# Optimization experiments

Measured on AMD Instinct MI355X. Metric: run time of the kernel, lower is better.

The kernel has to match this reference:

```python
import jax, jax.numpy as jnp
import numpy as np

B, C, H, W = 8, 512, 64, 64
C8 = C // 8

def setup_inputs() -> dict:
    key = jax.random.key(0)
    ks = jax.random.split(key, 10)
    rn = lambda k, shape: jax.random.normal(k, shape, jnp.float32)
    return {
        "q": rn(ks[0], (B, C, H, W)),
        "k": rn(ks[1], (B, C, H, W)),
        "v": rn(ks[2], (B, C, H, W)),
        "Wq": rn(ks[3], (C8, C)) * 0.05,
        "bq": rn(ks[4], (C8,)) * 0.05,
        "Wk": rn(ks[5], (C8, C)) * 0.05,
        "bk": rn(ks[6], (C8,)) * 0.05,
        "Wv": rn(ks[7], (C, C)) * 0.05,
        "bv": rn(ks[8], (C,)) * 0.05,
        "gamma": rn(ks[9], ()) * 0.05,
    }

def reference(q, k, v, Wq, bq, Wk, bk, Wv, bv, gamma):
    _, _, Hh, Ww = q.shape
    # 1x1 convs == per-pixel channel matmuls
    pq = jnp.einsum('oc,bchw->bohw', Wq, q) + bq[None, :, None, None]
    pk = jnp.einsum('oc,bchw->bohw', Wk, k) + bk[None, :, None, None]
    pv = jnp.einsum('oc,bchw->bohw', Wv, v) + bv[None, :, None, None]
    # column (height-axis) attention energies, diagonal masked to -inf
    eH = jnp.einsum('bchw,bckw->bhwk', pq, pk)  # [B,H,W,H]
    diag_mask = jnp.where(jnp.eye(Hh, dtype=bool), -jnp.inf, 0.0)  # [H,H]
    eH = eH + diag_mask[None, :, None, :]
    # row (width-axis) attention energies
    eW = jnp.einsum('bchw,bchk->bhwk', pq, pk)  # [B,H,W,W]
    # joint softmax over concatenated H+W candidates
    att = jax.nn.softmax(jnp.concatenate([eH, eW], axis=3), axis=3)
    aH, aW = att[..., :Hh], att[..., Hh:]
    outH = jnp.einsum('bckw,bhwk->bchw', pv, aH)
    outW = jnp.einsum('bchk,bhwk->bchw', pv, aW)
    return gamma * (outH + outW) + v
```

## Files before the change

### kernel.cpp

```cpp
#include <hip/hip_runtime.h>
#include <math.h>

#define Bz 8
#define Cc 512
#define Hh 64
#define Ww 64
#define HW 4096
#define BK 64
#define AS (BK + 4)
#define TS 68

typedef __attribute__((ext_vector_type(8))) short short8;
typedef __attribute__((ext_vector_type(4))) short short4v;
typedef __attribute__((ext_vector_type(4))) float floatx4;

__device__ inline unsigned short f2bf(float x) {
    unsigned u = __float_as_uint(x);
    return (unsigned short)((u + 0x7FFFu + ((u >> 16) & 1u)) >> 16);
}
__device__ inline float b2f(unsigned short h) {
    return __uint_as_float(((unsigned)h) << 16);
}
__device__ inline short8 ld8(const unsigned short* p) {
    short4v a = *(const short4v*)p;
    short4v b = *(const short4v*)(p + 4);
    short8 r;
    r[0]=a[0]; r[1]=a[1]; r[2]=a[2]; r[3]=a[3];
    r[4]=b[0]; r[5]=b[1]; r[6]=b[2]; r[7]=b[3];
    return r;
}
__device__ inline short8 ld8s(const unsigned short* base, int row, int koct) {
    return ld8(base + row * TS + (((koct ^ (row & 7))) << 3));
}

__global__ __launch_bounds__(256) void wconv_kernel(
    const float* __restrict__ Wq, const float* __restrict__ Wk,
    const float* __restrict__ Wv, unsigned short* __restrict__ wsc)
{
    const int i = blockIdx.x * 256 + threadIdx.x;
    if (i < 32768) {
        float x = Wq[i];
        unsigned short h = f2bf(x);
        wsc[i] = h;
        wsc[32768 + i] = f2bf(x - b2f(h));
    } else if (i < 65536) {
        int j = i - 32768;
        float x = Wk[j];
        unsigned short h = f2bf(x);
        wsc[65536 + j] = h;
        wsc[98304 + j] = f2bf(x - b2f(h));
    } else {
        int j = i - 65536;
        wsc[131072 + j] = f2bf(Wv[j]);
    }
}

__global__ __launch_bounds__(256, 4) void qkproj_kernel(
    const float* __restrict__ in0, const float* __restrict__ in1,
    const unsigned short* __restrict__ Wh0, const unsigned short* __restrict__ Wh1,
    const unsigned short* __restrict__ Wl0, const unsigned short* __restrict__ Wl1,
    const float* __restrict__ bias0, const float* __restrict__ bias1,
    float* __restrict__ out0, float* __restrict__ out1)
{
    __shared__ unsigned short Ah[2][64][AS];
    __shared__ unsigned short Bh[2][64][AS];
    const int sel = blockIdx.z >> 3;
    const int b   = blockIdx.z & 7;
    const float* __restrict__ in = sel ? in1 : in0;
    const unsigned short* __restrict__ Wh = sel ? Wh1 : Wh0;
    const unsigned short* __restrict__ Wl = sel ? Wl1 : Wl0;
    const float* __restrict__ bias = sel ? bias1 : bias0;
    float* __restrict__ outT = sel ? out1 : out0;

    const int t = threadIdx.x, lane = t & 63, wv = t >> 6;
    const int p0 = blockIdx.x * 64;
    const float* __restrict__ inb = in + (size_t)b * Cc * HW + p0;

    const int wm = (wv & 1) * 32;
    const int wn = (wv >> 1) * 32;

    floatx4 acc[2][2];
#pragma unroll
    for (int i = 0; i < 2; ++i)
#pragma unroll
        for (int j = 0; j < 2; ++j) acc[i][j] = (floatx4)0.f;

    const int pq4 = t & 15;
    const int cst = (t >> 4) * 4;

    for (int kt = 0; kt < Cc / BK; ++kt) {
        const int c0 = kt * BK;
        __syncthreads();
        float4 xq[4];
#pragma unroll
        for (int j = 0; j < 4; ++j)
            xq[j] = *(const float4*)(inb + (size_t)(c0 + cst + j) * HW + (pq4 << 2));
#pragma unroll
        for (int jj = 0; jj < 4; ++jj) {
            unsigned short h[4], l[4];
#pragma unroll
            for (int j = 0; j < 4; ++j) {
                float xx = ((const float*)&xq[j])[jj];
                h[j] = f2bf(xx);
                l[j] = f2bf(xx - b2f(h[j]));
            }
            *(ushort4*)&Ah[0][(pq4 << 2) + jj][cst] = make_ushort4(h[0], h[1], h[2], h[3]);
            *(ushort4*)&Ah[1][(pq4 << 2) + jj][cst] = make_ushort4(l[0], l[1], l[2], l[3]);
        }
#pragma unroll
        for (int r = 0; r < 2; ++r) {
            const int task = t + 256 * r;
            const int o = task >> 3, oct = task & 7;
            const unsigned short* srch = Wh + (size_t)o * Cc + c0 + oct * 8;
            const unsigned short* srcl = Wl + (size_t)o * Cc + c0 + oct * 8;
            *(ushort4*)&Bh[0][o][oct * 8]     = *(const ushort4*)srch;
            *(ushort4*)&Bh[0][o][oct * 8 + 4] = *(const ushort4*)(srch + 4);
            *(ushort4*)&Bh[1][o][oct * 8]     = *(const ushort4*)srcl;
            *(ushort4*)&Bh[1][o][oct * 8 + 4] = *(const ushort4*)(srcl + 4);
        }
        __syncthreads();
#pragma unroll
        for (int ks = 0; ks < 2; ++ks) {
            const int col = ks * 32 + (lane >> 4) * 8;
            short8 af[2], al[2], bfr[2], blr[2];
#pragma unroll
            for (int mt = 0; mt < 2; ++mt) {
                const int row = wm + mt * 16 + (lane & 15);
                af[mt] = ld8(&Ah[0][row][col]);
                al[mt] = ld8(&Ah[1][row][col]);
            }
#pragma unroll
            for (int nt = 0; nt < 2; ++nt) {
                const int row = wn + nt * 16 + (lane & 15);
                bfr[nt] = ld8(&Bh[0][row][col]);
                blr[nt] = ld8(&Bh[1][row][col]);
            }
#pragma unroll
            for (int mt = 0; mt < 2; ++mt)
#pragma unroll
                for (int nt = 0; nt < 2; ++nt) {
                    acc[mt][nt] = __builtin_amdgcn_mfma_f32_16x16x32_bf16(
                        af[mt], bfr[nt], acc[mt][nt], 0, 0, 0);
                    acc[mt][nt] = __builtin_amdgcn_mfma_f32_16x16x32_bf16(
                        al[mt], bfr[nt], acc[mt][nt], 0, 0, 0);
                    acc[mt][nt] = __builtin_amdgcn_mfma_f32_16x16x32_bf16(
                        af[mt], blr[nt], acc[mt][nt], 0, 0, 0);
                }
        }
    }
    const int oc = lane & 15, qd = lane >> 4;
#pragma unroll
    for (int nt = 0; nt < 2; ++nt) {
        const int o = wn + nt * 16 + oc;
        const float bs = bias[o];
#pragma unroll
        for (int mt = 0; mt < 2; ++mt)
#pragma unroll
            for (int r = 0; r < 4; ++r) {
                const int p = p0 + wm + mt * 16 + qd * 4 + r;
                outT[((size_t)b * HW + p) * 64 + o] = acc[mt][nt][r] + bs;
            }
    }
}

__global__ __launch_bounds__(256, 4) void vproj_kernel(
    const float* __restrict__ in, const unsigned short* __restrict__ Wh,
    const float* __restrict__ bias, unsigned short* __restrict__ out16)
{
    __shared__ unsigned short Ah[128][AS];
    __shared__ unsigned short Bh[128][AS];
    const int b = blockIdx.z;
    const int t = threadIdx.x, lane = t & 63, wv = t >> 6;
    const int p0 = blockIdx.x * 128, o0 = blockIdx.y * 128;
    const float* __restrict__ inb = in + (size_t)b * Cc * HW + p0;
    const int wm = (wv & 1) * 64, wn = (wv >> 1) * 64;

    floatx4 acc[4][4];
#pragma unroll
    for (int i = 0; i < 4; ++i)
#pragma unroll
        for (int j = 0; j < 4; ++j) acc[i][j] = (floatx4)0.f;

    const int pq4 = t & 31;
    const int oct = t >> 5;

    for (int kt = 0; kt < Cc / BK; ++kt) {
        const int c0 = kt * BK;
        __syncthreads();
#pragma unroll
        for (int half = 0; half < 2; ++half) {
            float4 xq[4];
#pragma unroll
            for (int j = 0; j < 4; ++j)
                xq[j] = *(const float4*)(inb + (size_t)(c0 + oct * 8 + half * 4 + j) * HW + (pq4 << 2));
#pragma unroll
            for (int jj = 0; jj < 4; ++jj) {
                unsigned short h[4];
#pragma unroll
                for (int j = 0; j < 4; ++j) h[j] = f2bf(((const float*)&xq[j])[jj]);
                *(ushort4*)&Ah[(pq4 << 2) + jj][oct * 8 + half * 4] =
                    make_ushort4(h[0], h[1], h[2], h[3]);
            }
        }
#pragma unroll
        for (int r = 0; r < 4; ++r) {
            const int task = t + 256 * r;
            const int o = task >> 3, oc8 = task & 7;
            const unsigned short* src = Wh + (size_t)(o0 + o) * Cc + c0 + oc8 * 8;
            *(ushort4*)&Bh[o][oc8 * 8]     = *(const ushort4*)src;
            *(ushort4*)&Bh[o][oc8 * 8 + 4] = *(const ushort4*)(src + 4);
        }
        __syncthreads();
#pragma unroll
        for (int ks = 0; ks < 2; ++ks) {
            const int col = ks * 32 + (lane >> 4) * 8;
            short8 af[4], bfr[4];
#pragma unroll
            for (int mt = 0; mt < 4; ++mt)
                af[mt] = ld8(&Ah[wm + mt * 16 + (lane & 15)][col]);
#pragma unroll
            for (int nt = 0; nt < 4; ++nt)
                bfr[nt] = ld8(&Bh[wn + nt * 16 + (lane & 15)][col]);
#pragma unroll
            for (int mt = 0; mt < 4; ++mt)
#pragma unroll
                for (int nt = 0; nt < 4; ++nt)
                    acc[mt][nt] = __builtin_amdgcn_mfma_f32_16x16x32_bf16(
                        af[mt], bfr[nt], acc[mt][nt], 0, 0, 0);
        }
    }
    const int oc = lane & 15, qd = lane >> 4;
#pragma unroll
    for (int nt = 0; nt < 4; ++nt) {
        const int o = o0 + wn + nt * 16 + oc;
        const float bs = bias[o];
#pragma unroll
        for (int mt = 0; mt < 4; ++mt)
#pragma unroll
            for (int r = 0; r < 4; ++r) {
                const int p = p0 + wm + mt * 16 + qd * 4 + r;
                out16[((size_t)b * HW + p) * 512 + o] = f2bf(acc[mt][nt][r] + bs);
            }
    }
}

__global__ __launch_bounds__(256) void scores_kernel(
    const float* __restrict__ pqT, const float* __restrict__ pkT,
    float* __restrict__ S)
{
    const int x    = blockIdx.x;
    const int b    = blockIdx.y;
    const int mode = blockIdx.z;
    __shared__ float Q[64][65];
    __shared__ float Kt[64][68];
    for (int idx = threadIdx.x; idx < 4096; idx += 256) {
        int r = idx >> 6, c = idx & 63;
        int p = mode ? (x * Ww + r) : (r * Ww + x);
        size_t g = ((size_t)b * HW + p) * 64 + c;
        Q[r][c] = pqT[g];
        Kt[c][r] = pkT[g];
    }
    __syncthreads();
    const int qr = threadIdx.x >> 2;
    const int k0 = (threadIdx.x & 3) * 16;
    float acc[16];
#pragma unroll
    for (int j = 0; j < 16; ++j) acc[j] = 0.f;
#pragma unroll 2
    for (int c = 0; c < 64; ++c) {
        const float qv = Q[qr][c];
        const float4 kv0 = *(const float4*)&Kt[c][k0];
        const float4 kv1 = *(const float4*)&Kt[c][k0 + 4];
        const float4 kv2 = *(const float4*)&Kt[c][k0 + 8];
        const float4 kv3 = *(const float4*)&Kt[c][k0 + 12];
        acc[0]  = fmaf(qv, kv0.x, acc[0]);
        acc[1]  = fmaf(qv, kv0.y, acc[1]);
        acc[2]  = fmaf(qv, kv0.z, acc[2]);
        acc[3]  = fmaf(qv, kv0.w, acc[3]);
        acc[4]  = fmaf(qv, kv1.x, acc[4]);
        acc[5]  = fmaf(qv, kv1.y, acc[5]);
        acc[6]  = fmaf(qv, kv1.z, acc[6]);
        acc[7]  = fmaf(qv, kv1.w, acc[7]);
        acc[8]  = fmaf(qv, kv2.x, acc[8]);
        acc[9]  = fmaf(qv, kv2.y, acc[9]);
        acc[10] = fmaf(qv, kv2.z, acc[10]);
        acc[11] = fmaf(qv, kv2.w, acc[11]);
        acc[12] = fmaf(qv, kv3.x, acc[12]);
        acc[13] = fmaf(qv, kv3.y, acc[13]);
        acc[14] = fmaf(qv, kv3.z, acc[14]);
        acc[15] = fmaf(qv, kv3.w, acc[15]);
    }
    size_t o = mode ? (((size_t)(b * Hh + x) * Ww + qr) * 128 + 64 + k0)
                    : (((size_t)(b * Hh + qr) * Ww + x) * 128 + k0);
#pragma unroll
    for (int j = 0; j < 16; ++j) S[o + j] = acc[j];
}

__global__ __launch_bounds__(256) void softmax_kernel(
    const float* __restrict__ S, unsigned short* __restrict__ Abf)
{
    const int wave = threadIdx.x >> 6;
    const int lane = threadIdx.x & 63;
    const size_t row = (size_t)blockIdx.x * 4 + wave;
    const int h = (int)((row / Ww) % Hh);
    const float* p = S + row * 128;
    float s0 = p[lane], s1 = p[lane + 64];
    if (lane == h) s0 = -INFINITY;
    float m = fmaxf(s0, s1);
#pragma unroll
    for (int off = 32; off > 0; off >>= 1) m = fmaxf(m, __shfl_xor(m, off));
    float e0 = __expf(s0 - m), e1 = __expf(s1 - m);
    float s = e0 + e1;
#pragma unroll
    for (int off = 32; off > 0; off >>= 1) s += __shfl_xor(s, off);
    float inv = 1.0f / s;
    Abf[row * 128 + lane]      = f2bf(e0 * inv);
    Abf[row * 128 + 64 + lane] = f2bf(e1 * inv);
}

__global__ __launch_bounds__(256) void outH_mfma_kernel(
    const unsigned short* __restrict__ Abf, const unsigned short* __restrict__ pvT16,
    unsigned short* __restrict__ TH16)
{
    const int w = blockIdx.x;
    const int ctg = blockIdx.y;
    const int b = blockIdx.z;
    const int t = threadIdx.x, lane = t & 63, wv = t >> 6;
    const int l15 = lane & 15, h4 = lane >> 4;
    __shared__ unsigned short A[64 * TS];
    __shared__ unsigned short Pt[64 * TS];

    {
        const int rr = t >> 2, kq = t & 3;
        const unsigned short* src = Abf + ((((size_t)b * Hh + rr) * Ww + w) << 7) + kq * 16;
        ushort4 a0 = *(const ushort4*)(src);
        ushort4 a1 = *(const ushort4*)(src + 4);
        ushort4 a2 = *(const ushort4*)(src + 8);
        ushort4 a3 = *(const ushort4*)(src + 12);
        const int sw = (rr & 7) << 3;
        const int q0 = rr * TS + (((kq * 2) << 3) ^ sw);
        const int q1 = rr * TS + (((kq * 2 + 1) << 3) ^ sw);
        *(ushort4*)&A[q0] = a0; *(ushort4*)&A[q0 + 4] = a1;
        *(ushort4*)&A[q1] = a2; *(ushort4*)&A[q1 + 4] = a3;
    }
    __syncthreads();
    const int hm = (wv & 1) * 32, cn = (wv >> 1) * 32;
    short8 ah[2][2];
#pragma unroll
    for (int mt = 0; mt < 2; ++mt)
#pragma unroll
        for (int ks = 0; ks < 2; ++ks)
            ah[mt][ks] = ld8s(A, hm + mt * 16 + l15, ks * 4 + h4);

    for (int cc = 0; cc < 2; ++cc) {
        const int cbase = (ctg * 2 + cc) * 64;
        __syncthreads();
        {
            const int kp = t >> 3, co = t & 7, k0 = kp * 2;
            const unsigned short* s0 = pvT16 + (((size_t)b * HW + (size_t)k0 * Ww + w) << 9) + cbase + co * 8;
            const unsigned short* s1 = s0 + ((size_t)Ww << 9);
            short8 r0 = *(const short8*)s0;
            short8 r1 = *(const short8*)s1;
            const int oct = k0 >> 3, klo = k0 & 7;
#pragma unroll
            for (int j = 0; j < 8; ++j) {
                const int c = co * 8 + j;
                unsigned vv = (unsigned)(unsigned short)r0[j] | ((unsigned)(unsigned short)r1[j] << 16);
                *(unsigned*)&Pt[c * TS + (((oct ^ (c & 7)) << 3) + klo)] = vv;
            }
        }
        __syncthreads();
        floatx4 acc[2][2];
#pragma unroll
        for (int i = 0; i < 2; ++i)
#pragma unroll
            for (int j = 0; j < 2; ++j) acc[i][j] = (floatx4)0.f;
        short8 pf[2][2];
#pragma unroll
        for (int nt = 0; nt < 2; ++nt)
#pragma unroll
            for (int ks = 0; ks < 2; ++ks)
                pf[nt][ks] = ld8s(Pt, cn + nt * 16 + l15, ks * 4 + h4);
#pragma unroll
        for (int ks = 0; ks < 2; ++ks)
#pragma unroll
            for (int mt = 0; mt < 2; ++mt)
#pragma unroll
                for (int nt = 0; nt < 2; ++nt)
                    acc[mt][nt] = __builtin_amdgcn_mfma_f32_16x16x32_bf16(
                        ah[mt][ks], pf[nt][ks], acc[mt][nt], 0, 0, 0);
        const int quad = lane >> 4, oc = lane & 15;
#pragma unroll
        for (int mt = 0; mt < 2; ++mt)
#pragma unroll
            for (int nt = 0; nt < 2; ++nt) {
                const int c = cn + nt * 16 + oc;
                unsigned short* dst = TH16 + ((((size_t)b * Ww + w) * Hh) << 9) + cbase + c;
#pragma unroll
                for (int r = 0; r < 4; ++r) {
                    const int hh = hm + mt * 16 + quad * 4 + r;
                    dst[(size_t)hh << 9] = f2bf(acc[mt][nt][r]);
                }
            }
    }
}

__global__ __launch_bounds__(256) void outW_mfma_kernel(
    const unsigned short* __restrict__ Abf, const unsigned short* __restrict__ pvT16,
    const unsigned short* __restrict__ TH16, const float* __restrict__ vin,
    const float* __restrict__ gamma_p, float* __restrict__ out)
{
    const int h = blockIdx.x;
    const int ctg = blockIdx.y;
    const int b = blockIdx.z;
    const int t = threadIdx.x, lane = t & 63, wv = t >> 6;
    const int l15 = lane & 15, h4 = lane >> 4;
    const float gamma = gamma_p[0];
    __shared__ unsigned short A[64 * TS];
    __shared__ unsigned short Pt[64 * TS];
    __shared__ unsigned short T2[64 * TS];

    {
        const int rr = t >> 2, kq = t & 3;
        const unsigned short* src = Abf + ((((size_t)b * Hh + h) * Ww + rr) << 7) + 64 + kq * 16;
        ushort4 a0 = *(const ushort4*)(src);
        ushort4 a1 = *(const ushort4*)(src + 4);
        ushort4 a2 = *(const ushort4*)(src + 8);
        ushort4 a3 = *(const ushort4*)(src + 12);
        const int sw = (rr & 7) << 3;
        const int q0 = rr * TS + (((kq * 2) << 3) ^ sw);
        const int q1 = rr * TS + (((kq * 2 + 1) << 3) ^ sw);
        *(ushort4*)&A[q0] = a0; *(ushort4*)&A[q0 + 4] = a1;
        *(ushort4*)&A[q1] = a2; *(ushort4*)&A[q1 + 4] = a3;
    }
    __syncthreads();
    const int cm = (wv & 1) * 32, wn = (wv >> 1) * 32;
    short8 aw[2][2];
#pragma unroll
    for (int nt = 0; nt < 2; ++nt)
#pragma unroll
        for (int ks = 0; ks < 2; ++ks)
            aw[nt][ks] = ld8s(A, wn + nt * 16 + l15, ks * 4 + h4);

    for (int cc = 0; cc < 2; ++cc) {
        const int cbase = (ctg * 2 + cc) * 64;
        __syncthreads();
        {
            const int kp = t >> 3, co = t & 7, k0 = kp * 2;
            const unsigned short* s0 = pvT16 + (((size_t)b * HW + (size_t)h * Ww + k0) << 9) + cbase + co * 8;
            const unsigned short* s1 = s0 + 512;
            short8 r0 = *(const short8*)s0;
            short8 r1 = *(const short8*)s1;
            const int oct = k0 >> 3, klo = k0 & 7;
#pragma unroll
            for (int j = 0; j < 8; ++j) {
                const int c = co * 8 + j;
                unsigned vv = (unsigned)(unsigned short)r0[j] | ((unsigned)(unsigned short)r1[j] << 16);
                *(unsigned*)&Pt[c * TS + (((oct ^ (c & 7)) << 3) + klo)] = vv;
            }
        }
        {
            const int wr = t >> 2, cq = t & 3;
            const unsigned short* src = TH16 + ((((size_t)b * Ww + wr) * Hh + h) << 9) + cbase + cq * 16;
            short8 t0 = *(const short8*)src;
            short8 t1 = *(const short8*)(src + 8);
#pragma unroll
            for (int j = 0; j < 4; ++j) {
                unsigned va = (unsigned)(unsigned short)t0[2 * j] | ((unsigned)(unsigned short)t0[2 * j + 1] << 16);
                *(unsigned*)&T2[wr * TS + cq * 16 + 2 * j] = va;
                unsigned vb = (unsigned)(unsigned short)t1[2 * j] | ((unsigned)(unsigned short)t1[2 * j + 1] << 16);
                *(unsigned*)&T2[wr * TS + cq * 16 + 8 + 2 * j] = vb;
            }
        }
        __syncthreads();
        floatx4 acc[2][2];
#pragma unroll
        for (int i = 0; i < 2; ++i)
#pragma unroll
            for (int j = 0; j < 2; ++j) acc[i][j] = (floatx4)0.f;
        short8 pf[2][2];
#pragma unroll
        for (int mt = 0; mt < 2; ++mt)
#pragma unroll
            for (int ks = 0; ks < 2; ++ks)
                pf[mt][ks] = ld8s(Pt, cm + mt * 16 + l15, ks * 4 + h4);
#pragma unroll
        for (int ks = 0; ks < 2; ++ks)
#pragma unroll
            for (int mt = 0; mt < 2; ++mt)
#pragma unroll
                for (int nt = 0; nt < 2; ++nt)
                    acc[mt][nt] = __builtin_amdgcn_mfma_f32_16x16x32_bf16(
                        pf[mt][ks], aw[nt][ks], acc[mt][nt], 0, 0, 0);
        const int quad = lane >> 4, oc = lane & 15;
#pragma unroll
        for (int mt = 0; mt < 2; ++mt)
#pragma unroll
            for (int nt = 0; nt < 2; ++nt) {
                const int wcol = wn + nt * 16 + oc;
#pragma unroll
                for (int r = 0; r < 4; ++r) {
                    const int c = cm + mt * 16 + quad * 4 + r;
                    const float t2v = b2f(T2[wcol * TS + c]);
                    const size_t oa = ((size_t)(b * Cc + cbase + c) * HW) + (size_t)h * Ww + wcol;
                    out[oa] = gamma * (acc[mt][nt][r] + t2v) + vin[oa];
                }
            }
    }
}

extern "C" void kernel_launch(void* const* d_in, const int* in_sizes, int n_in,
                              void* d_out, int out_size, void* d_ws, size_t ws_size,
                              hipStream_t stream)
{
    const float* q   = (const float*)d_in[0];
    const float* k   = (const float*)d_in[1];
    const float* v   = (const float*)d_in[2];
    const float* Wq  = (const float*)d_in[3];
    const float* bq  = (const float*)d_in[4];
    const float* Wk  = (const float*)d_in[5];
    const float* bk  = (const float*)d_in[6];
    const float* Wv  = (const float*)d_in[7];
    const float* bv  = (const float*)d_in[8];
    const float* gam = (const float*)d_in[9];
    float* out = (float*)d_out;
    float* ws  = (float*)d_ws;

    float* pqT = ws;
    float* pkT = ws + 2097152;
    unsigned short* pvT16 = (unsigned short*)(ws + 4194304);
    float* S   = ws + 12582912;
    unsigned short* Abf  = (unsigned short*)(ws + 16777216);
    unsigned short* TH16 = (unsigned short*)(ws + 18874368);

    unsigned short* wsc = (unsigned short*)S;
    const unsigned short* Wqh = wsc;
    const unsigned short* Wql = wsc + 32768;
    const unsigned short* Wkh = wsc + 65536;
    const unsigned short* Wkl = wsc + 98304;
    const unsigned short* Wvh = wsc + 131072;

    wconv_kernel<<<1280, 256, 0, stream>>>(Wq, Wk, Wv, wsc);
    qkproj_kernel<<<dim3(64, 1, 16), 256, 0, stream>>>(
        q, k, Wqh, Wkh, Wql, Wkl, bq, bk, pqT, pkT);
    vproj_kernel<<<dim3(32, 4, 8), 256, 0, stream>>>(v, Wvh, bv, pvT16);
    scores_kernel<<<dim3(64, 8, 2), 256, 0, stream>>>(pqT, pkT, S);
    softmax_kernel<<<8192, 256, 0, stream>>>(S, Abf);
    outH_mfma_kernel<<<dim3(64, 4, 8), 256, 0, stream>>>(Abf, pvT16, TH16);
    outW_mfma_kernel<<<dim3(64, 4, 8), 256, 0, stream>>>(Abf, pvT16, TH16, v, gam, out);
}
```

Measured before the change: 332.3 us.

## Register-prefetch next K tile in projections and add column-major pv copy for outH

The qk and v projection kernels now load the next K tile of inputs and weights into registers while MFMAs run on the current shared-memory tile, which hides global-load latency. The v projection tile shrinks from 128 to 64 pixels, doubling the grid. It also writes a second bf16 copy of pv in a [b][w][h][c] layout so outH reads contiguous rows instead of striding by width. This costs extra write bandwidth and 32MB more workspace, plus more register pressure from the prefetch buffers.

```diff
diff --git a/kernel.cpp b/kernel.cpp
--- a/kernel.cpp
+++ b/kernel.cpp
@@ -87,20 +87,35 @@
 
     const int pq4 = t & 15;
     const int cst = (t >> 4) * 4;
-
-    for (int kt = 0; kt < Cc / BK; ++kt) {
+    const int bo  = t >> 3;
+    const int boc = t & 7;
+
+    float4  xa[4];
+    ushort4 wbh[2][2], wbl[2][2];
+
+    auto qload = [&](int kt) {
         const int c0 = kt * BK;
-        __syncthreads();
-        float4 xq[4];
 #pragma unroll
         for (int j = 0; j < 4; ++j)
-            xq[j] = *(const float4*)(inb + (size_t)(c0 + cst + j) * HW + (pq4 << 2));
+            xa[j] = *(const float4*)(inb + (size_t)(c0 + cst + j) * HW + (pq4 << 2));
+#pragma unroll
+        for (int r = 0; r < 2; ++r) {
+            const int o = bo + 32 * r;
+            const unsigned short* srch = Wh + (size_t)o * Cc + c0 + boc * 8;
+            const unsigned short* srcl = Wl + (size_t)o * Cc + c0 + boc * 8;
+            wbh[r][0] = *(const ushort4*)srch;
+            wbh[r][1] = *(const ushort4*)(srch + 4);
+            wbl[r][0] = *(const ushort4*)srcl;
+            wbl[r][1] = *(const ushort4*)(srcl + 4);
+        }
+    };
+    auto qstore = [&]() {
 #pragma unroll
         for (int jj = 0; jj < 4; ++jj) {
             unsigned short h[4], l[4];
 #pragma unroll
             for (int j = 0; j < 4; ++j) {
-                float xx = ((const float*)&xq[j])[jj];
+                float xx = ((const float*)&xa[j])[jj];
                 h[j] = f2bf(xx);
                 l[j] = f2bf(xx - b2f(h[j]));
             }
@@ -109,16 +124,19 @@
         }
 #pragma unroll
         for (int r = 0; r < 2; ++r) {
-            const int task = t + 256 * r;
-            const int o = task >> 3, oct = task & 7;
-            const unsigned short* srch = Wh + (size_t)o * Cc + c0 + oct * 8;
-            const unsigned short* srcl = Wl + (size_t)o * Cc + c0 + oct * 8;
-            *(ushort4*)&Bh[0][o][oct * 8]     = *(const ushort4*)srch;
-            *(ushort4*)&Bh[0][o][oct * 8 + 4] = *(const ushort4*)(srch + 4);
-            *(ushort4*)&Bh[1][o][oct * 8]     = *(const ushort4*)srcl;
-            *(ushort4*)&Bh[1][o][oct * 8 + 4] = *(const ushort4*)(srcl + 4);
-        }
-        __syncthreads();
+            const int o = bo + 32 * r;
+            *(ushort4*)&Bh[0][o][boc * 8]     = wbh[r][0];
+            *(ushort4*)&Bh[0][o][boc * 8 + 4] = wbh[r][1];
+            *(ushort4*)&Bh[1][o][boc * 8]     = wbl[r][0];
+            *(ushort4*)&Bh[1][o][boc * 8 + 4] = wbl[r][1];
+        }
+    };
+
+    qload(0);
+    qstore();
+    __syncthreads();
+    for (int kt = 0; kt < Cc / BK; ++kt) {
+        if (kt + 1 < Cc / BK) qload(kt + 1);
 #pragma unroll
         for (int ks = 0; ks < 2; ++ks) {
             const int col = ks * 32 + (lane >> 4) * 8;
@@ -147,6 +165,8 @@
                         af[mt], blr[nt], acc[mt][nt], 0, 0, 0);
                 }
         }
+        __syncthreads();
+        if (kt + 1 < Cc / BK) { qstore(); __syncthreads(); }
     }
     const int oc = lane & 15, qd = lane >> 4;
 #pragma unroll
@@ -165,81 +185,97 @@
 
 __global__ __launch_bounds__(256, 4) void vproj_kernel(
     const float* __restrict__ in, const unsigned short* __restrict__ Wh,
-    const float* __restrict__ bias, unsigned short* __restrict__ out16)
-{
-    __shared__ unsigned short Ah[128][AS];
+    const float* __restrict__ bias, unsigned short* __restrict__ pvT16,
+    unsigned short* __restrict__ pvH16)
+{
+    __shared__ unsigned short Ah[64][AS];
     __shared__ unsigned short Bh[128][AS];
     const int b = blockIdx.z;
     const int t = threadIdx.x, lane = t & 63, wv = t >> 6;
-    const int p0 = blockIdx.x * 128, o0 = blockIdx.y * 128;
+    const int p0 = blockIdx.x * 64, o0 = blockIdx.y * 128;
     const float* __restrict__ inb = in + (size_t)b * Cc * HW + p0;
-    const int wm = (wv & 1) * 64, wn = (wv >> 1) * 64;
-
-    floatx4 acc[4][4];
-#pragma unroll
-    for (int i = 0; i < 4; ++i)
+    const int wm = (wv & 1) * 32, wn = (wv >> 1) * 64;
+
+    floatx4 acc[2][4];
+#pragma unroll
+    for (int i = 0; i < 2; ++i)
 #pragma unroll
         for (int j = 0; j < 4; ++j) acc[i][j] = (floatx4)0.f;
 
-    const int pq4 = t & 31;
-    const int oct = t >> 5;
-
+    const int pq4 = t & 15;
+    const int cst = (t >> 4) * 4;
+    const int bo  = t >> 3;
+    const int boc = t & 7;
+
+    float4  xa[4];
+    ushort4 wb[4][2];
+
+    auto vload = [&](int kt) {
+        const int c0 = kt * BK;
+#pragma unroll
+        for (int j = 0; j < 4; ++j)
+            xa[j] = *(const float4*)(inb + (size_t)(c0 + cst + j) * HW + (pq4 << 2));
+#pragma unroll
+        for (int r = 0; r < 4; ++r) {
+            const unsigned short* src = Wh + (size_t)(o0 + bo + 32 * r) * Cc + c0 + boc * 8;
+            wb[r][0] = *(const ushort4*)src;
+            wb[r][1] = *(const ushort4*)(src + 4);
+        }
+    };
+    auto vstore = [&]() {
+#pragma unroll
+        for (int jj = 0; jj < 4; ++jj) {
+            unsigned short h[4];
+#pragma unroll
+            for (int j = 0; j < 4; ++j) h[j] = f2bf(((const float*)&xa[j])[jj]);
+            *(ushort4*)&Ah[(pq4 << 2) + jj][cst] = make_ushort4(h[0], h[1], h[2], h[3]);
+        }
+#pragma unroll
+        for (int r = 0; r < 4; ++r) {
+            *(ushort4*)&Bh[bo + 32 * r][boc * 8]     = wb[r][0];
+            *(ushort4*)&Bh[bo + 32 * r][boc * 8 + 4] = wb[r][1];
+        }
+    };
+
+    vload(0);
+    vstore();
+    __syncthreads();
     for (int kt = 0; kt < Cc / BK; ++kt) {
-        const int c0 = kt * BK;
-        __syncthreads();
-#pragma unroll
-        for (int half = 0; half < 2; ++half) {
-            float4 xq[4];
-#pragma unroll
-            for (int j = 0; j < 4; ++j)
-                xq[j] = *(const float4*)(inb + (size_t)(c0 + oct * 8 + half * 4 + j) * HW + (pq4 << 2));
-#pragma unroll
-            for (int jj = 0; jj < 4; ++jj) {
-                unsigned short h[4];
-#pragma unroll
-                for (int j = 0; j < 4; ++j) h[j] = f2bf(((const float*)&xq[j])[jj]);
-                *(ushort4*)&Ah[(pq4 << 2) + jj][oct * 8 + half * 4] =
-                    make_ushort4(h[0], h[1], h[2], h[3]);
-            }
-        }
-#pragma unroll
-        for (int r = 0; r < 4; ++r) {
-            const int task = t + 256 * r;
-            const int o = task >> 3, oc8 = task & 7;
-            const unsigned short* src = Wh + (size_t)(o0 + o) * Cc + c0 + oc8 * 8;
-            *(ushort4*)&Bh[o][oc8 * 8]     = *(const ushort4*)src;
-            *(ushort4*)&Bh[o][oc8 * 8 + 4] = *(const ushort4*)(src + 4);
-        }
-        __syncthreads();
+        if (kt + 1 < Cc / BK) vload(kt + 1);
 #pragma unroll
         for (int ks = 0; ks < 2; ++ks) {
             const int col = ks * 32 + (lane >> 4) * 8;
-            short8 af[4], bfr[4];
-#pragma unroll
-            for (int mt = 0; mt < 4; ++mt)
+            short8 af[2], bfr[4];
+#pragma unroll
+            for (int mt = 0; mt < 2; ++mt)
                 af[mt] = ld8(&Ah[wm + mt * 16 + (lane & 15)][col]);
 #pragma unroll
             for (int nt = 0; nt < 4; ++nt)
                 bfr[nt] = ld8(&Bh[wn + nt * 16 + (lane & 15)][col]);
 #pragma unroll
-            for (int mt = 0; mt < 4; ++mt)
+            for (int mt = 0; mt < 2; ++mt)
 #pragma unroll
                 for (int nt = 0; nt < 4; ++nt)
                     acc[mt][nt] = __builtin_amdgcn_mfma_f32_16x16x32_bf16(
                         af[mt], bfr[nt], acc[mt][nt], 0, 0, 0);
         }
+        __syncthreads();
+        if (kt + 1 < Cc / BK) { vstore(); __syncthreads(); }
     }
     const int oc = lane & 15, qd = lane >> 4;
+    const int kk = p0 >> 6;
 #pragma unroll
     for (int nt = 0; nt < 4; ++nt) {
         const int o = o0 + wn + nt * 16 + oc;
         const float bs = bias[o];
 #pragma unroll
-        for (int mt = 0; mt < 4; ++mt)
+        for (int mt = 0; mt < 2; ++mt)
 #pragma unroll
             for (int r = 0; r < 4; ++r) {
-                const int p = p0 + wm + mt * 16 + qd * 4 + r;
-                out16[((size_t)b * HW + p) * 512 + o] = f2bf(acc[mt][nt][r] + bs);
+                const int pw = wm + mt * 16 + qd * 4 + r;
+                const unsigned short val = f2bf(acc[mt][nt][r] + bs);
+                pvT16[((size_t)b * HW + p0 + pw) * 512 + o] = val;
+                pvH16[(((size_t)b * Ww + pw) * Hh + kk) * 512 + o] = val;
             }
     }
 }
@@ -319,7 +355,7 @@
 }
 
 __global__ __launch_bounds__(256) void outH_mfma_kernel(
-    const unsigned short* __restrict__ Abf, const unsigned short* __restrict__ pvT16,
+    const unsigned short* __restrict__ Abf, const unsigned short* __restrict__ pvH16,
     unsigned short* __restrict__ TH16)
 {
     const int w = blockIdx.x;
@@ -356,12 +392,12 @@
         const int cbase = (ctg * 2 + cc) * 64;
         __syncthreads();
         {
-            const int kp = t >> 3, co = t & 7, k0 = kp * 2;
-            const unsigned short* s0 = pvT16 + (((size_t)b * HW + (size_t)k0 * Ww + w) << 9) + cbase + co * 8;
-            const unsigned short* s1 = s0 + ((size_t)Ww << 9);
+            const int kp = t >> 3, co = t & 7, k0v = kp * 2;
+            const unsigned short* s0 = pvH16 + ((((size_t)b * Ww + w) * Hh + k0v) << 9) + cbase + co * 8;
+            const unsigned short* s1 = s0 + 512;
             short8 r0 = *(const short8*)s0;
             short8 r1 = *(const short8*)s1;
-            const int oct = k0 >> 3, klo = k0 & 7;
+            const int oct = k0v >> 3, klo = k0v & 7;
 #pragma unroll
             for (int j = 0; j < 8; ++j) {
                 const int c = co * 8 + j;
@@ -532,6 +568,7 @@
     float* S   = ws + 12582912;
     unsigned short* Abf  = (unsigned short*)(ws + 16777216);
     unsigned short* TH16 = (unsigned short*)(ws + 18874368);
+    unsigned short* pvH16 = (unsigned short*)(ws + 27262976);
 
     unsigned short* wsc = (unsigned short*)S;
     const unsigned short* Wqh = wsc;
@@ -543,9 +580,9 @@
     wconv_kernel<<<1280, 256, 0, stream>>>(Wq, Wk, Wv, wsc);
     qkproj_kernel<<<dim3(64, 1, 16), 256, 0, stream>>>(
         q, k, Wqh, Wkh, Wql, Wkl, bq, bk, pqT, pkT);
-    vproj_kernel<<<dim3(32, 4, 8), 256, 0, stream>>>(v, Wvh, bv, pvT16);
+    vproj_kernel<<<dim3(64, 4, 8), 256, 0, stream>>>(v, Wvh, bv, pvT16, pvH16);
     scores_kernel<<<dim3(64, 8, 2), 256, 0, stream>>>(pqT, pkT, S);
     softmax_kernel<<<8192, 256, 0, stream>>>(S, Abf);
-    outH_mfma_kernel<<<dim3(64, 4, 8), 256, 0, stream>>>(Abf, pvT16, TH16);
+    outH_mfma_kernel<<<dim3(64, 4, 8), 256, 0, stream>>>(Abf, pvH16, TH16);
     outW_mfma_kernel<<<dim3(64, 4, 8), 256, 0, stream>>>(Abf, pvT16, TH16, v, gam, out);
 }
```

Result: no change. 332.6 us (+0.1%).

## Load weights directly from global, shrink vproj tiles, add transposed pv copy

Applied to the files above, without the earlier changes.

The qk and v projection kernels stop staging weight tiles in LDS and instead read MFMA B fragments straight from global memory, which frees shared memory and allows higher occupancy hints. The v projection drops from 128x128 to 64x64 tiles with more blocks. It also writes a second (b,w,h,c)-ordered bf16 copy of pv so the outH kernel reads contiguous rows along h instead of strided ones. In exchange it uses extra workspace and write bandwidth for the duplicate pv, and fetches weights from global memory repeatedly rather than reusing them through LDS.

```diff
diff --git a/kernel.cpp b/kernel.cpp
--- a/kernel.cpp
+++ b/kernel.cpp
@@ -55,7 +55,7 @@
     }
 }
 
-__global__ __launch_bounds__(256, 4) void qkproj_kernel(
+__global__ __launch_bounds__(256, 8) void qkproj_kernel(
     const float* __restrict__ in0, const float* __restrict__ in1,
     const unsigned short* __restrict__ Wh0, const unsigned short* __restrict__ Wh1,
     const unsigned short* __restrict__ Wl0, const unsigned short* __restrict__ Wl1,
@@ -63,7 +63,6 @@
     float* __restrict__ out0, float* __restrict__ out1)
 {
     __shared__ unsigned short Ah[2][64][AS];
-    __shared__ unsigned short Bh[2][64][AS];
     const int sel = blockIdx.z >> 3;
     const int b   = blockIdx.z & 7;
     const float* __restrict__ in = sel ? in1 : in0;
@@ -73,6 +72,7 @@
     float* __restrict__ outT = sel ? out1 : out0;
 
     const int t = threadIdx.x, lane = t & 63, wv = t >> 6;
+    const int l15 = lane & 15, h4 = lane >> 4;
     const int p0 = blockIdx.x * 64;
     const float* __restrict__ inb = in + (size_t)b * Cc * HW + p0;
 
@@ -107,33 +107,23 @@
             *(ushort4*)&Ah[0][(pq4 << 2) + jj][cst] = make_ushort4(h[0], h[1], h[2], h[3]);
             *(ushort4*)&Ah[1][(pq4 << 2) + jj][cst] = make_ushort4(l[0], l[1], l[2], l[3]);
         }
-#pragma unroll
-        for (int r = 0; r < 2; ++r) {
-            const int task = t + 256 * r;
-            const int o = task >> 3, oct = task & 7;
-            const unsigned short* srch = Wh + (size_t)o * Cc + c0 + oct * 8;
-            const unsigned short* srcl = Wl + (size_t)o * Cc + c0 + oct * 8;
-            *(ushort4*)&Bh[0][o][oct * 8]     = *(const ushort4*)srch;
-            *(ushort4*)&Bh[0][o][oct * 8 + 4] = *(const ushort4*)(srch + 4);
-            *(ushort4*)&Bh[1][o][oct * 8]     = *(const ushort4*)srcl;
-            *(ushort4*)&Bh[1][o][oct * 8 + 4] = *(const ushort4*)(srcl + 4);
-        }
         __syncthreads();
 #pragma unroll
         for (int ks = 0; ks < 2; ++ks) {
-            const int col = ks * 32 + (lane >> 4) * 8;
+            const int col  = ks * 32 + h4 * 8;
+            const int colc = c0 + col;
             short8 af[2], al[2], bfr[2], blr[2];
 #pragma unroll
+            for (int nt = 0; nt < 2; ++nt) {
+                const int o = wn + nt * 16 + l15;
+                bfr[nt] = *(const short8*)(Wh + (size_t)o * Cc + colc);
+                blr[nt] = *(const short8*)(Wl + (size_t)o * Cc + colc);
+            }
+#pragma unroll
             for (int mt = 0; mt < 2; ++mt) {
-                const int row = wm + mt * 16 + (lane & 15);
+                const int row = wm + mt * 16 + l15;
                 af[mt] = ld8(&Ah[0][row][col]);
                 al[mt] = ld8(&Ah[1][row][col]);
-            }
-#pragma unroll
-            for (int nt = 0; nt < 2; ++nt) {
-                const int row = wn + nt * 16 + (lane & 15);
-                bfr[nt] = ld8(&Bh[0][row][col]);
-                blr[nt] = ld8(&Bh[1][row][col]);
             }
 #pragma unroll
             for (int mt = 0; mt < 2; ++mt)
@@ -163,83 +153,76 @@
     }
 }
 
-__global__ __launch_bounds__(256, 4) void vproj_kernel(
+__global__ __launch_bounds__(256, 8) void vproj_kernel(
     const float* __restrict__ in, const unsigned short* __restrict__ Wh,
-    const float* __restrict__ bias, unsigned short* __restrict__ out16)
-{
-    __shared__ unsigned short Ah[128][AS];
-    __shared__ unsigned short Bh[128][AS];
+    const float* __restrict__ bias, unsigned short* __restrict__ pvT16,
+    unsigned short* __restrict__ pvH16)
+{
+    __shared__ unsigned short Ah[64][AS];
     const int b = blockIdx.z;
     const int t = threadIdx.x, lane = t & 63, wv = t >> 6;
-    const int p0 = blockIdx.x * 128, o0 = blockIdx.y * 128;
+    const int l15 = lane & 15, h4 = lane >> 4;
+    const int p0 = blockIdx.x * 64, o0 = blockIdx.y * 64;
     const float* __restrict__ inb = in + (size_t)b * Cc * HW + p0;
-    const int wm = (wv & 1) * 64, wn = (wv >> 1) * 64;
-
-    floatx4 acc[4][4];
-#pragma unroll
-    for (int i = 0; i < 4; ++i)
-#pragma unroll
-        for (int j = 0; j < 4; ++j) acc[i][j] = (floatx4)0.f;
-
-    const int pq4 = t & 31;
-    const int oct = t >> 5;
+    const int wm = (wv & 1) * 32, wn = (wv >> 1) * 32;
+
+    floatx4 acc[2][2];
+#pragma unroll
+    for (int i = 0; i < 2; ++i)
+#pragma unroll
+        for (int j = 0; j < 2; ++j) acc[i][j] = (floatx4)0.f;
+
+    const int pq4 = t & 15;
+    const int cst = (t >> 4) * 4;
 
     for (int kt = 0; kt < Cc / BK; ++kt) {
         const int c0 = kt * BK;
         __syncthreads();
-#pragma unroll
-        for (int half = 0; half < 2; ++half) {
-            float4 xq[4];
-#pragma unroll
-            for (int j = 0; j < 4; ++j)
-                xq[j] = *(const float4*)(inb + (size_t)(c0 + oct * 8 + half * 4 + j) * HW + (pq4 << 2));
-#pragma unroll
-            for (int jj = 0; jj < 4; ++jj) {
-                unsigned short h[4];
-#pragma unroll
-                for (int j = 0; j < 4; ++j) h[j] = f2bf(((const float*)&xq[j])[jj]);
-                *(ushort4*)&Ah[(pq4 << 2) + jj][oct * 8 + half * 4] =
-                    make_ushort4(h[0], h[1], h[2], h[3]);
-            }
-        }
-#pragma unroll
-        for (int r = 0; r < 4; ++r) {
-            const int task = t + 256 * r;
-            const int o = task >> 3, oc8 = task & 7;
-            const unsigned short* src = Wh + (size_t)(o0 + o) * Cc + c0 + oc8 * 8;
-            *(ushort4*)&Bh[o][oc8 * 8]     = *(const ushort4*)src;
-            *(ushort4*)&Bh[o][oc8 * 8 + 4] = *(const ushort4*)(src + 4);
+        float4 xq[4];
+#pragma unroll
+        for (int j = 0; j < 4; ++j)
+            xq[j] = *(const float4*)(inb + (size_t)(c0 + cst + j) * HW + (pq4 << 2));
+#pragma unroll
+        for (int jj = 0; jj < 4; ++jj) {
+            unsigned short h[4];
+#pragma unroll
+            for (int j = 0; j < 4; ++j) h[j] = f2bf(((const float*)&xq[j])[jj]);
+            *(ushort4*)&Ah[(pq4 << 2) + jj][cst] = make_ushort4(h[0], h[1], h[2], h[3]);
         }
         __syncthreads();
 #pragma unroll
         for (int ks = 0; ks < 2; ++ks) {
-            const int col = ks * 32 + (lane >> 4) * 8;
-            short8 af[4], bfr[4];
-#pragma unroll
-            for (int mt = 0; mt < 4; ++mt)
-                af[mt] = ld8(&Ah[wm + mt * 16 + (lane & 15)][col]);
-#pragma unroll
-            for (int nt = 0; nt < 4; ++nt)
-                bfr[nt] = ld8(&Bh[wn + nt * 16 + (lane & 15)][col]);
-#pragma unroll
-            for (int mt = 0; mt < 4; ++mt)
-#pragma unroll
-                for (int nt = 0; nt < 4; ++nt)
+            const int col  = ks * 32 + h4 * 8;
+            const int colc = c0 + col;
+            short8 af[2], bfr[2];
+#pragma unroll
+            for (int nt = 0; nt < 2; ++nt)
+                bfr[nt] = *(const short8*)(Wh + (size_t)(o0 + wn + nt * 16 + l15) * Cc + colc);
+#pragma unroll
+            for (int mt = 0; mt < 2; ++mt)
+                af[mt] = ld8(&Ah[wm + mt * 16 + l15][col]);
+#pragma unroll
+            for (int mt = 0; mt < 2; ++mt)
+#pragma unroll
+                for (int nt = 0; nt < 2; ++nt)
                     acc[mt][nt] = __builtin_amdgcn_mfma_f32_16x16x32_bf16(
                         af[mt], bfr[nt], acc[mt][nt], 0, 0, 0);
         }
     }
     const int oc = lane & 15, qd = lane >> 4;
-#pragma unroll
-    for (int nt = 0; nt < 4; ++nt) {
+    const int kk = blockIdx.x;
+#pragma unroll
+    for (int nt = 0; nt < 2; ++nt) {
         const int o = o0 + wn + nt * 16 + oc;
         const float bs = bias[o];
 #pragma unroll
-        for (int mt = 0; mt < 4; ++mt)
+        for (int mt = 0; mt < 2; ++mt)
 #pragma unroll
             for (int r = 0; r < 4; ++r) {
-                const int p = p0 + wm + mt * 16 + qd * 4 + r;
-                out16[((size_t)b * HW + p) * 512 + o] = f2bf(acc[mt][nt][r] + bs);
+                const int pw = wm + mt * 16 + qd * 4 + r;
+                const unsigned short val = f2bf(acc[mt][nt][r] + bs);
+                pvT16[((size_t)b * HW + p0 + pw) * 512 + o] = val;
+                pvH16[(((size_t)b * Ww + pw) * Hh + kk) * 512 + o] = val;
             }
     }
 }
@@ -319,7 +302,7 @@
 }
 
 __global__ __launch_bounds__(256) void outH_mfma_kernel(
-    const unsigned short* __restrict__ Abf, const unsigned short* __restrict__ pvT16,
+    const unsigned short* __restrict__ Abf, const unsigned short* __restrict__ pvH16,
     unsigned short* __restrict__ TH16)
 {
     const int w = blockIdx.x;
@@ -356,12 +339,12 @@
         const int cbase = (ctg * 2 + cc) * 64;
         __syncthreads();
         {
-            const int kp = t >> 3, co = t & 7, k0 = kp * 2;
-            const unsigned short* s0 = pvT16 + (((size_t)b * HW + (size_t)k0 * Ww + w) << 9) + cbase + co * 8;
-            const unsigned short* s1 = s0 + ((size_t)Ww << 9);
+            const int kp = t >> 3, co = t & 7, k0v = kp * 2;
+            const unsigned short* s0 = pvH16 + ((((size_t)b * Ww + w) * Hh + k0v) << 9) + cbase + co * 8;
+            const unsigned short* s1 = s0 + 512;
             short8 r0 = *(const short8*)s0;
             short8 r1 = *(const short8*)s1;
-            const int oct = k0 >> 3, klo = k0 & 7;
+            const int oct = k0v >> 3, klo = k0v & 7;
 #pragma unroll
             for (int j = 0; j < 8; ++j) {
                 const int c = co * 8 + j;
@@ -532,6 +515,7 @@
     float* S   = ws + 12582912;
     unsigned short* Abf  = (unsigned short*)(ws + 16777216);
     unsigned short* TH16 = (unsigned short*)(ws + 18874368);
+    unsigned short* pvH16 = (unsigned short*)(ws + 27262976);
 
     unsigned short* wsc = (unsigned short*)S;
     const unsigned short* Wqh = wsc;
@@ -543,9 +527,9 @@
     wconv_kernel<<<1280, 256, 0, stream>>>(Wq, Wk, Wv, wsc);
     qkproj_kernel<<<dim3(64, 1, 16), 256, 0, stream>>>(
         q, k, Wqh, Wkh, Wql, Wkl, bq, bk, pqT, pkT);
-    vproj_kernel<<<dim3(32, 4, 8), 256, 0, stream>>>(v, Wvh, bv, pvT16);
+    vproj_kernel<<<dim3(64, 8, 8), 256, 0, stream>>>(v, Wvh, bv, pvT16, pvH16);
     scores_kernel<<<dim3(64, 8, 2), 256, 0, stream>>>(pqT, pkT, S);
     softmax_kernel<<<8192, 256, 0, stream>>>(S, Abf);
-    outH_mfma_kernel<<<dim3(64, 4, 8), 256, 0, stream>>>(Abf, pvT16, TH16);
+    outH_mfma_kernel<<<dim3(64, 4, 8), 256, 0, stream>>>(Abf, pvH16, TH16);
     outW_mfma_kernel<<<dim3(64, 4, 8), 256, 0, stream>>>(Abf, pvT16, TH16, v, gam, out);
 }
```

After: 384.3 us. 1.16x slower.
